# Kernel tuning notes

Measured on AMD Instinct MI355X. Metric: run time of the kernel, lower is better.

## Reference

```python
import jax, jax.numpy as jnp
import numpy as np

N_NODES = 50000


def _gcn_norm(edge_index, num_nodes):
    """PyG GCNConv normalization: add self-loops, symmetric deg^{-1/2} weights."""
    loops = jnp.arange(num_nodes, dtype=edge_index.dtype)
    src = jnp.concatenate([edge_index[0], loops])
    dst = jnp.concatenate([edge_index[1], loops])
    deg = jax.ops.segment_sum(jnp.ones_like(dst, dtype=jnp.float32), dst,
                              num_segments=num_nodes)
    dinv = jax.lax.rsqrt(jnp.maximum(deg, 1.0))  # self-loops guarantee deg>=1
    norm = dinv[src] * dinv[dst]                 # [E + N]
    return src, dst, norm


def _gcn_conv(x, W, b, src, dst, norm, num_nodes):
    h = x @ W                                    # [N, out] dense GEMM
    msg = h[src] * norm[:, None]                 # gather + scale
    agg = jax.ops.segment_sum(msg, dst, num_segments=num_nodes)
    return agg + b


def setup_inputs() -> dict:
    key = jax.random.key(0)
    ks = jax.random.split(key, 8)
    d = 128
    scale = 1.0 / np.sqrt(d)
    emb = jax.random.normal(ks[0], (N_NODES, d), dtype=jnp.float32)
    W1 = jax.random.normal(ks[1], (d, d), dtype=jnp.float32) * scale
    W2 = jax.random.normal(ks[2], (d, d), dtype=jnp.float32) * scale
    W3 = jax.random.normal(ks[3], (d, d), dtype=jnp.float32) * scale
    b1 = jnp.zeros((d,), dtype=jnp.float32)
    b2 = jnp.zeros((d,), dtype=jnp.float32)
    b3 = jnp.zeros((d,), dtype=jnp.float32)
    edge_index = jax.random.randint(ks[4], (2, 600000), 0, N_NODES, dtype=jnp.int64)
    return {"emb": emb, "W1": W1, "b1": b1, "W2": W2, "b2": b2,
            "W3": W3, "b3": b3, "edge_index": edge_index}


def reference(emb, W1, b1, W2, b2, W3, b3, edge_index):
    # Eval-mode forward: F.dropout(training=False) is identity.
    src, dst, norm = _gcn_norm(edge_index, N_NODES)
    x = emb
    x = jax.nn.relu(_gcn_conv(x, W1, b1, src, dst, norm, N_NODES))
    x = jax.nn.relu(_gcn_conv(x, W2, b2, src, dst, norm, N_NODES))
    x = _gcn_conv(x, W3, b3, src, dst, norm, N_NODES)
    x = x.at[0].set(0.0)  # x[0] = zeros(x.shape[1])
    return x
```

## Files before the change

kernel.cpp:

```cpp
#include <hip/hip_runtime.h>
#include <hip/hip_fp16.h>

#define NN 50000
#define D 128
#define STRIDE 64

typedef __attribute__((ext_vector_type(16))) float f32x16;
typedef _Float16 h16;
typedef __attribute__((ext_vector_type(8))) _Float16 h16x8;

struct alignas(16) H8 { h16 h[8]; };

typedef const __attribute__((address_space(1))) void gvoid;
typedef __attribute__((address_space(3))) void lvoid;

__global__ __launch_bounds__(256) void wprep_kernel(const float* __restrict__ W1,
                                                    const float* __restrict__ W2,
                                                    const float* __restrict__ W3,
                                                    h16* __restrict__ Wsp,
                                                    int* __restrict__ cnt) {
    const int b  = blockIdx.x;
    const int w  = b >> 3;
    const int ks = b & 7;
    const float* W = w == 0 ? W1 : (w == 1 ? W2 : W3);
    h16* dst = Wsp + w * 32768;
    const int l  = threadIdx.x & 63;
    const int ct = threadIdx.x >> 6;
    const int n  = ct * 32 + (l & 31);
    const int lh = l >> 5;
    const int kbase = ks * 16 + lh * 8;
    H8 hi8, lo8;
#pragma unroll
    for (int j = 0; j < 8; j++) {
        float wv = W[(kbase + j) * D + n];
        h16 hi = (h16)wv;
        hi8.h[j] = hi;
        lo8.h[j] = (h16)(wv - (float)hi);
    }
    const int base = ((ks * 4 + ct) * 64 + l) * 8;
    *(H8*)(dst + base)         = hi8;
    *(H8*)(dst + base + 16384) = lo8;
    for (int i = b * 256 + threadIdx.x; i < NN; i += 24 * 256) cnt[i] = 0;
}

__global__ __launch_bounds__(256) void fill_kernel(const int* __restrict__ srcA,
                                                   const int* __restrict__ dstA,
                                                   int* __restrict__ cnt,
                                                   int* __restrict__ slots, int noct) {
    int t = blockIdx.x * 256 + threadIdx.x;
    if (t >= noct) return;
    int4 sa = ((const int4*)srcA)[2 * t];
    int4 sb = ((const int4*)srcA)[2 * t + 1];
    int4 da = ((const int4*)dstA)[2 * t];
    int4 db = ((const int4*)dstA)[2 * t + 1];
    int p0 = atomicAdd(&cnt[da.x], 1);
    int p1 = atomicAdd(&cnt[da.y], 1);
    int p2 = atomicAdd(&cnt[da.z], 1);
    int p3 = atomicAdd(&cnt[da.w], 1);
    int p4 = atomicAdd(&cnt[db.x], 1);
    int p5 = atomicAdd(&cnt[db.y], 1);
    int p6 = atomicAdd(&cnt[db.z], 1);
    int p7 = atomicAdd(&cnt[db.w], 1);
    if (p0 < STRIDE - 4) slots[da.x * STRIDE + p0] = sa.x;
    if (p1 < STRIDE - 4) slots[da.y * STRIDE + p1] = sa.y;
    if (p2 < STRIDE - 4) slots[da.z * STRIDE + p2] = sa.z;
    if (p3 < STRIDE - 4) slots[da.w * STRIDE + p3] = sa.w;
    if (p4 < STRIDE - 4) slots[db.x * STRIDE + p4] = sb.x;
    if (p5 < STRIDE - 4) slots[db.y * STRIDE + p5] = sb.y;
    if (p6 < STRIDE - 4) slots[db.z * STRIDE + p6] = sb.z;
    if (p7 < STRIDE - 4) slots[db.w * STRIDE + p7] = sb.w;
}

__global__ __launch_bounds__(256, 2) void gemm_mfma(const void* __restrict__ Xv, int x_is_f32,
                                                    const h16* __restrict__ Wsp,
                                                    h16* __restrict__ H, int M) {
    __shared__ h16 Ws[32768];
    {
        const int t = threadIdx.x;
#pragma unroll
        for (int i = 0; i < 16; i++) {
            const int off = (i * 256 + t) * 8;
            __builtin_amdgcn_global_load_lds((gvoid*)(Wsp + off), (lvoid*)(Ws + off),
                                             16, 0, 0);
        }
    }
    __syncthreads();

    const int wave = threadIdx.x >> 6;
    const int lane = threadIdx.x & 63;
    const int row0 = blockIdx.x * 128 + wave * 32;
    const int arow = min(row0 + (lane & 31), M - 1);
    const int koff = (lane >> 5) * 8;

    f32x16 acc[4] = {};

#pragma unroll
    for (int ks = 0; ks < 8; ks++) {
        h16x8 ahi, alo;
        if (x_is_f32) {
            const float* p = (const float*)Xv + (size_t)arow * D + koff + ks * 16;
            float4 fa = *(const float4*)p;
            float4 fb = *(const float4*)(p + 4);
            float f[8] = {fa.x, fa.y, fa.z, fa.w, fb.x, fb.y, fb.z, fb.w};
#pragma unroll
            for (int j = 0; j < 8; j++) {
                h16 hi = (h16)f[j];
                ahi[j] = hi;
                alo[j] = (h16)(f[j] - (float)hi);
            }
        } else {
            const h16* p = (const h16*)Xv + (size_t)arow * D + koff + ks * 16;
            ahi = *(const h16x8*)p;
        }
#pragma unroll
        for (int ct = 0; ct < 4; ct++) {
            const int base = ((ks * 4 + ct) * 64 + lane) * 8;
            h16x8 bhi = *(const h16x8*)(Ws + base);
            h16x8 blo = *(const h16x8*)(Ws + base + 16384);
            acc[ct] = __builtin_amdgcn_mfma_f32_32x32x16_f16(ahi, bhi, acc[ct], 0, 0, 0);
            acc[ct] = __builtin_amdgcn_mfma_f32_32x32x16_f16(ahi, blo, acc[ct], 0, 0, 0);
            if (x_is_f32)
                acc[ct] = __builtin_amdgcn_mfma_f32_32x32x16_f16(alo, bhi, acc[ct], 0, 0, 0);
        }
    }

    __syncthreads();
    {
        h16* C_lds = Ws;
        const int col0 = lane & 31;
        const int lr0  = 4 * (lane >> 5);
#pragma unroll
        for (int ct = 0; ct < 4; ct++) {
#pragma unroll
            for (int r = 0; r < 16; r++) {
                const int lrow = lr0 + (r & 3) + 8 * (r >> 2);
                C_lds[(wave * 32 + lrow) * D + ct * 32 + col0] = (h16)acc[ct][r];
            }
        }
        const h16* src = C_lds + wave * 32 * D;
        h16* gdst = H + (size_t)row0 * D;
#pragma unroll
        for (int j = 0; j < 8; j++) {
            const int i = j * 64 + lane;
            const int row = row0 + (i >> 4);
            if (row < M)
                *(h16x8*)(gdst + (size_t)i * 8) = *(const h16x8*)(src + i * 8);
        }
    }
}

__global__ __launch_bounds__(256) void agg_kernel(const h16* __restrict__ H,
                                                  const int* __restrict__ cnt,
                                                  const int* __restrict__ slots,
                                                  const float* __restrict__ bias,
                                                  h16* __restrict__ out16,
                                                  float* __restrict__ out32,
                                                  int mode) {
    const int lane = threadIdx.x & 63;
    const int node = blockIdx.x * 4 + (threadIdx.x >> 6);
    const int q    = lane >> 4;
    const int col  = (lane & 15) * 8;

    const int c = __builtin_amdgcn_readfirstlane(cnt[node]);
    const float di = rsqrtf((float)c + 1.0f);
    const int sbase = node * STRIDE;
    const int pc = min((c + 8) & ~7, STRIDE);

    float aA[8] = {0.f, 0.f, 0.f, 0.f, 0.f, 0.f, 0.f, 0.f};
    float aB[8] = {0.f, 0.f, 0.f, 0.f, 0.f, 0.f, 0.f, 0.f};

    int sa = slots[sbase + q];
    int sb = slots[sbase + 4 + q];

    for (int p = 0; p < pc; p += 8) {
        int sa_n = slots[sbase + min(p + 8 + q, STRIDE - 1)];
        int sb_n = slots[sbase + min(p + 12 + q, STRIDE - 1)];
        const int ja = p + q;
        const int jb = p + 4 + q;
        const int ca = (ja < c) ? sa : node;
        const int cb = (jb < c) ? sb : node;
        float wa = (ja < c) ? rsqrtf((float)cnt[ca] + 1.0f) : ((ja == c) ? di : 0.f);
        float wb = (jb < c) ? rsqrtf((float)cnt[cb] + 1.0f) : ((jb == c) ? di : 0.f);
        h16x8 va = *(const h16x8*)(H + (size_t)ca * D + col);
        h16x8 vb = *(const h16x8*)(H + (size_t)cb * D + col);
#pragma unroll
        for (int j = 0; j < 8; j++) {
            aA[j] = fmaf(wa, (float)va[j], aA[j]);
            aB[j] = fmaf(wb, (float)vb[j], aB[j]);
        }
        sa = sa_n; sb = sb_n;
    }

#pragma unroll
    for (int j = 0; j < 8; j++) {
        float v = aA[j] + aB[j];
        v += __shfl_xor(v, 16, 64);
        v += __shfl_xor(v, 32, 64);
        aA[j] = v;
    }

    if (lane < 16) {
        float4 bb0 = *(const float4*)(bias + col);
        float4 bb1 = *(const float4*)(bias + col + 4);
        float r[8];
        r[0] = fmaf(di, aA[0], bb0.x); r[1] = fmaf(di, aA[1], bb0.y);
        r[2] = fmaf(di, aA[2], bb0.z); r[3] = fmaf(di, aA[3], bb0.w);
        r[4] = fmaf(di, aA[4], bb1.x); r[5] = fmaf(di, aA[5], bb1.y);
        r[6] = fmaf(di, aA[6], bb1.z); r[7] = fmaf(di, aA[7], bb1.w);
        if (mode == 0) {
            h16x8 o;
#pragma unroll
            for (int j = 0; j < 8; j++) o[j] = (h16)fmaxf(r[j], 0.f);
            *(h16x8*)(out16 + (size_t)node * D + col) = o;
        } else {
            if (node == 0) {
#pragma unroll
                for (int j = 0; j < 8; j++) r[j] = 0.f;
            }
            *(float4*)(out32 + (size_t)node * D + col)     = make_float4(r[0], r[1], r[2], r[3]);
            *(float4*)(out32 + (size_t)node * D + col + 4) = make_float4(r[4], r[5], r[6], r[7]);
        }
    }
}


extern "C" void kernel_launch(void* const* d_in, const int* in_sizes, int n_in,
                              void* d_out, int out_size, void* d_ws, size_t ws_size,
                              hipStream_t stream) {
    const float* emb = (const float*)d_in[0];
    const float* W1  = (const float*)d_in[1];
    const float* b1  = (const float*)d_in[2];
    const float* W2  = (const float*)d_in[3];
    const float* b2  = (const float*)d_in[4];
    const float* W3  = (const float*)d_in[5];
    const float* b3  = (const float*)d_in[6];
    const int*   ei  = (const int*)d_in[7];

    const int E = in_sizes[7] / 2;
    const int* srcA = ei;
    const int* dstA = ei + E;
    float* out = (float*)d_out;

    char* ws = (char*)d_ws;
    size_t off = 0;
    auto alloc = [&](size_t bytes) -> void* {
        void* p = ws + off;
        off = (off + bytes + 255) & ~(size_t)255;
        return p;
    };
    h16* h      = (h16*)alloc((size_t)NN * D * 2);
    h16* x16    = (h16*)alloc((size_t)NN * D * 2);
    int* cnt    = (int*)alloc((size_t)NN * 4);
    int* slots  = (int*)alloc((size_t)NN * STRIDE * 4);
    h16* Wsp    = (h16*)alloc((size_t)3 * 32768 * 2);

    const int T = 256;
    const int gemm_grid = (NN + 127) / 128;
    const int agg_grid  = NN / 4;
    const int noct = E / 8;

    wprep_kernel<<<24, T, 0, stream>>>(W1, W2, W3, Wsp, cnt);
    gemm_mfma<<<gemm_grid, T, 0, stream>>>(emb, 1, Wsp, h, NN);
    fill_kernel<<<(noct + T - 1) / T, T, 0, stream>>>(srcA, dstA, cnt, slots, noct);
    agg_kernel<<<agg_grid, T, 0, stream>>>(h, cnt, slots, b1, x16, nullptr, 0);
    gemm_mfma<<<gemm_grid, T, 0, stream>>>(x16, 0, Wsp + 32768, h, NN);
    agg_kernel<<<agg_grid, T, 0, stream>>>(h, cnt, slots, b2, x16, nullptr, 0);
    gemm_mfma<<<gemm_grid, T, 0, stream>>>(x16, 0, Wsp + 65536, h, NN);
    agg_kernel<<<agg_grid, T, 0, stream>>>(h, cnt, slots, b3, nullptr, out, 1);
}
```

Measured before the change: 252.1 us.

## Fuse edge-slot fill into first GEMM, enlarge GEMM blocks, batch agg nodes

The separate fill kernel is removed. Its atomic bucketing of edges by destination now runs at the tail of the first GEMM launch, saving one launch. The GEMM moves to 512-thread blocks covering 256 rows, with launch bounds of (512, 4). The aggregation kernel now has each wave process four nodes in turn and hoists the bias load. Risks: the tighter launch bound may force register spills for the 64-float accumulators, and fewer, larger agg blocks may hide memory latency less well.

```diff
diff --git a/kernel.cpp b/kernel.cpp
--- a/kernel.cpp
+++ b/kernel.cpp
@@ -43,43 +43,19 @@
     for (int i = b * 256 + threadIdx.x; i < NN; i += 24 * 256) cnt[i] = 0;
 }
 
-__global__ __launch_bounds__(256) void fill_kernel(const int* __restrict__ srcA,
-                                                   const int* __restrict__ dstA,
-                                                   int* __restrict__ cnt,
-                                                   int* __restrict__ slots, int noct) {
-    int t = blockIdx.x * 256 + threadIdx.x;
-    if (t >= noct) return;
-    int4 sa = ((const int4*)srcA)[2 * t];
-    int4 sb = ((const int4*)srcA)[2 * t + 1];
-    int4 da = ((const int4*)dstA)[2 * t];
-    int4 db = ((const int4*)dstA)[2 * t + 1];
-    int p0 = atomicAdd(&cnt[da.x], 1);
-    int p1 = atomicAdd(&cnt[da.y], 1);
-    int p2 = atomicAdd(&cnt[da.z], 1);
-    int p3 = atomicAdd(&cnt[da.w], 1);
-    int p4 = atomicAdd(&cnt[db.x], 1);
-    int p5 = atomicAdd(&cnt[db.y], 1);
-    int p6 = atomicAdd(&cnt[db.z], 1);
-    int p7 = atomicAdd(&cnt[db.w], 1);
-    if (p0 < STRIDE - 4) slots[da.x * STRIDE + p0] = sa.x;
-    if (p1 < STRIDE - 4) slots[da.y * STRIDE + p1] = sa.y;
-    if (p2 < STRIDE - 4) slots[da.z * STRIDE + p2] = sa.z;
-    if (p3 < STRIDE - 4) slots[da.w * STRIDE + p3] = sa.w;
-    if (p4 < STRIDE - 4) slots[db.x * STRIDE + p4] = sb.x;
-    if (p5 < STRIDE - 4) slots[db.y * STRIDE + p5] = sb.y;
-    if (p6 < STRIDE - 4) slots[db.z * STRIDE + p6] = sb.z;
-    if (p7 < STRIDE - 4) slots[db.w * STRIDE + p7] = sb.w;
-}
-
-__global__ __launch_bounds__(256, 2) void gemm_mfma(const void* __restrict__ Xv, int x_is_f32,
+__global__ __launch_bounds__(512, 4) void gemm_mfma(const void* __restrict__ Xv, int x_is_f32,
                                                     const h16* __restrict__ Wsp,
-                                                    h16* __restrict__ H, int M) {
+                                                    h16* __restrict__ H, int M,
+                                                    const int* __restrict__ srcA,
+                                                    const int* __restrict__ dstA,
+                                                    int* __restrict__ cnt,
+                                                    int* __restrict__ slots, int noct) {
     __shared__ h16 Ws[32768];
     {
         const int t = threadIdx.x;
 #pragma unroll
-        for (int i = 0; i < 16; i++) {
-            const int off = (i * 256 + t) * 8;
+        for (int i = 0; i < 8; i++) {
+            const int off = (i * 512 + t) * 8;
             __builtin_amdgcn_global_load_lds((gvoid*)(Wsp + off), (lvoid*)(Ws + off),
                                              16, 0, 0);
         }
@@ -88,7 +64,7 @@
 
     const int wave = threadIdx.x >> 6;
     const int lane = threadIdx.x & 63;
-    const int row0 = blockIdx.x * 128 + wave * 32;
+    const int row0 = blockIdx.x * 256 + wave * 32;
     const int arow = min(row0 + (lane & 31), M - 1);
     const int koff = (lane >> 5) * 8;
 
@@ -147,6 +123,32 @@
                 *(h16x8*)(gdst + (size_t)i * 8) = *(const h16x8*)(src + i * 8);
         }
     }
+
+    if (srcA) {
+        int t = blockIdx.x * 512 + threadIdx.x;
+        if (t < noct) {
+            int4 sa = ((const int4*)srcA)[2 * t];
+            int4 sb = ((const int4*)srcA)[2 * t + 1];
+            int4 da = ((const int4*)dstA)[2 * t];
+            int4 db = ((const int4*)dstA)[2 * t + 1];
+            int p0 = atomicAdd(&cnt[da.x], 1);
+            int p1 = atomicAdd(&cnt[da.y], 1);
+            int p2 = atomicAdd(&cnt[da.z], 1);
+            int p3 = atomicAdd(&cnt[da.w], 1);
+            int p4 = atomicAdd(&cnt[db.x], 1);
+            int p5 = atomicAdd(&cnt[db.y], 1);
+            int p6 = atomicAdd(&cnt[db.z], 1);
+            int p7 = atomicAdd(&cnt[db.w], 1);
+            if (p0 < STRIDE - 4) slots[da.x * STRIDE + p0] = sa.x;
+            if (p1 < STRIDE - 4) slots[da.y * STRIDE + p1] = sa.y;
+            if (p2 < STRIDE - 4) slots[da.z * STRIDE + p2] = sa.z;
+            if (p3 < STRIDE - 4) slots[da.w * STRIDE + p3] = sa.w;
+            if (p4 < STRIDE - 4) slots[db.x * STRIDE + p4] = sb.x;
+            if (p5 < STRIDE - 4) slots[db.y * STRIDE + p5] = sb.y;
+            if (p6 < STRIDE - 4) slots[db.z * STRIDE + p6] = sb.z;
+            if (p7 < STRIDE - 4) slots[db.w * STRIDE + p7] = sb.w;
+        }
+    }
 }
 
 __global__ __launch_bounds__(256) void agg_kernel(const h16* __restrict__ H,
@@ -156,69 +158,73 @@
                                                   h16* __restrict__ out16,
                                                   float* __restrict__ out32,
                                                   int mode) {
-    const int lane = threadIdx.x & 63;
-    const int node = blockIdx.x * 4 + (threadIdx.x >> 6);
-    const int q    = lane >> 4;
-    const int col  = (lane & 15) * 8;
-
-    const int c = __builtin_amdgcn_readfirstlane(cnt[node]);
-    const float di = rsqrtf((float)c + 1.0f);
-    const int sbase = node * STRIDE;
-    const int pc = min((c + 8) & ~7, STRIDE);
-
-    float aA[8] = {0.f, 0.f, 0.f, 0.f, 0.f, 0.f, 0.f, 0.f};
-    float aB[8] = {0.f, 0.f, 0.f, 0.f, 0.f, 0.f, 0.f, 0.f};
-
-    int sa = slots[sbase + q];
-    int sb = slots[sbase + 4 + q];
-
-    for (int p = 0; p < pc; p += 8) {
-        int sa_n = slots[sbase + min(p + 8 + q, STRIDE - 1)];
-        int sb_n = slots[sbase + min(p + 12 + q, STRIDE - 1)];
-        const int ja = p + q;
-        const int jb = p + 4 + q;
-        const int ca = (ja < c) ? sa : node;
-        const int cb = (jb < c) ? sb : node;
-        float wa = (ja < c) ? rsqrtf((float)cnt[ca] + 1.0f) : ((ja == c) ? di : 0.f);
-        float wb = (jb < c) ? rsqrtf((float)cnt[cb] + 1.0f) : ((jb == c) ? di : 0.f);
-        h16x8 va = *(const h16x8*)(H + (size_t)ca * D + col);
-        h16x8 vb = *(const h16x8*)(H + (size_t)cb * D + col);
+    const int lane  = threadIdx.x & 63;
+    const int q     = lane >> 4;
+    const int col   = (lane & 15) * 8;
+    const int node0 = blockIdx.x * 16 + (threadIdx.x >> 6) * 4;
+
+    const float4 bb0 = *(const float4*)(bias + col);
+    const float4 bb1 = *(const float4*)(bias + col + 4);
+
+    for (int nn = 0; nn < 4; nn++) {
+        const int node = node0 + nn;
+        const int c = __builtin_amdgcn_readfirstlane(cnt[node]);
+        const float di = rsqrtf((float)c + 1.0f);
+        const int sbase = node * STRIDE;
+        const int pc = min((c + 8) & ~7, STRIDE);
+
+        float aA[8] = {0.f, 0.f, 0.f, 0.f, 0.f, 0.f, 0.f, 0.f};
+        float aB[8] = {0.f, 0.f, 0.f, 0.f, 0.f, 0.f, 0.f, 0.f};
+
+        int sa = slots[sbase + q];
+        int sb = slots[sbase + 4 + q];
+
+        for (int p = 0; p < pc; p += 8) {
+            int sa_n = slots[sbase + min(p + 8 + q, STRIDE - 1)];
+            int sb_n = slots[sbase + min(p + 12 + q, STRIDE - 1)];
+            const int ja = p + q;
+            const int jb = p + 4 + q;
+            const int ca = (ja < c) ? sa : node;
+            const int cb = (jb < c) ? sb : node;
+            float wa = (ja < c) ? rsqrtf((float)cnt[ca] + 1.0f) : ((ja == c) ? di : 0.f);
+            float wb = (jb < c) ? rsqrtf((float)cnt[cb] + 1.0f) : ((jb == c) ? di : 0.f);
+            h16x8 va = *(const h16x8*)(H + (size_t)ca * D + col);
+            h16x8 vb = *(const h16x8*)(H + (size_t)cb * D + col);
+#pragma unroll
+            for (int j = 0; j < 8; j++) {
+                aA[j] = fmaf(wa, (float)va[j], aA[j]);
+                aB[j] = fmaf(wb, (float)vb[j], aB[j]);
+            }
+            sa = sa_n; sb = sb_n;
+        }
+
 #pragma unroll
         for (int j = 0; j < 8; j++) {
-            aA[j] = fmaf(wa, (float)va[j], aA[j]);
-            aB[j] = fmaf(wb, (float)vb[j], aB[j]);
-        }
-        sa = sa_n; sb = sb_n;
-    }
-
-#pragma unroll
-    for (int j = 0; j < 8; j++) {
-        float v = aA[j] + aB[j];
-        v += __shfl_xor(v, 16, 64);
-        v += __shfl_xor(v, 32, 64);
-        aA[j] = v;
-    }
-
-    if (lane < 16) {
-        float4 bb0 = *(const float4*)(bias + col);
-        float4 bb1 = *(const float4*)(bias + col + 4);
-        float r[8];
-        r[0] = fmaf(di, aA[0], bb0.x); r[1] = fmaf(di, aA[1], bb0.y);
-        r[2] = fmaf(di, aA[2], bb0.z); r[3] = fmaf(di, aA[3], bb0.w);
-        r[4] = fmaf(di, aA[4], bb1.x); r[5] = fmaf(di, aA[5], bb1.y);
-        r[6] = fmaf(di, aA[6], bb1.z); r[7] = fmaf(di, aA[7], bb1.w);
-        if (mode == 0) {
-            h16x8 o;
-#pragma unroll
-            for (int j = 0; j < 8; j++) o[j] = (h16)fmaxf(r[j], 0.f);
-            *(h16x8*)(out16 + (size_t)node * D + col) = o;
-        } else {
-            if (node == 0) {
-#pragma unroll
-                for (int j = 0; j < 8; j++) r[j] = 0.f;
-            }
-            *(float4*)(out32 + (size_t)node * D + col)     = make_float4(r[0], r[1], r[2], r[3]);
-            *(float4*)(out32 + (size_t)node * D + col + 4) = make_float4(r[4], r[5], r[6], r[7]);
+            float v = aA[j] + aB[j];
+            v += __shfl_xor(v, 16, 64);
+            v += __shfl_xor(v, 32, 64);
+            aA[j] = v;
+        }
+
+        if (lane < 16) {
+            float r[8];
+            r[0] = fmaf(di, aA[0], bb0.x); r[1] = fmaf(di, aA[1], bb0.y);
+            r[2] = fmaf(di, aA[2], bb0.z); r[3] = fmaf(di, aA[3], bb0.w);
+            r[4] = fmaf(di, aA[4], bb1.x); r[5] = fmaf(di, aA[5], bb1.y);
+            r[6] = fmaf(di, aA[6], bb1.z); r[7] = fmaf(di, aA[7], bb1.w);
+            if (mode == 0) {
+                h16x8 o;
+#pragma unroll
+                for (int j = 0; j < 8; j++) o[j] = (h16)fmaxf(r[j], 0.f);
+                *(h16x8*)(out16 + (size_t)node * D + col) = o;
+            } else {
+                if (node == 0) {
+#pragma unroll
+                    for (int j = 0; j < 8; j++) r[j] = 0.f;
+                }
+                *(float4*)(out32 + (size_t)node * D + col)     = make_float4(r[0], r[1], r[2], r[3]);
+                *(float4*)(out32 + (size_t)node * D + col + 4) = make_float4(r[4], r[5], r[6], r[7]);
+            }
         }
     }
 }
@@ -254,17 +260,18 @@
     int* slots  = (int*)alloc((size_t)NN * STRIDE * 4);
     h16* Wsp    = (h16*)alloc((size_t)3 * 32768 * 2);
 
-    const int T = 256;
-    const int gemm_grid = (NN + 127) / 128;
-    const int agg_grid  = NN / 4;
+    const int gemm_grid = (NN + 255) / 256;
+    const int agg_grid  = NN / 16;
     const int noct = E / 8;
 
-    wprep_kernel<<<24, T, 0, stream>>>(W1, W2, W3, Wsp, cnt);
-    gemm_mfma<<<gemm_grid, T, 0, stream>>>(emb, 1, Wsp, h, NN);
-    fill_kernel<<<(noct + T - 1) / T, T, 0, stream>>>(srcA, dstA, cnt, slots, noct);
-    agg_kernel<<<agg_grid, T, 0, stream>>>(h, cnt, slots, b1, x16, nullptr, 0);
-    gemm_mfma<<<gemm_grid, T, 0, stream>>>(x16, 0, Wsp + 32768, h, NN);
-    agg_kernel<<<agg_grid, T, 0, stream>>>(h, cnt, slots, b2, x16, nullptr, 0);
-    gemm_mfma<<<gemm_grid, T, 0, stream>>>(x16, 0, Wsp + 65536, h, NN);
-    agg_kernel<<<agg_grid, T, 0, stream>>>(h, cnt, slots, b3, nullptr, out, 1);
-}
+    wprep_kernel<<<24, 256, 0, stream>>>(W1, W2, W3, Wsp, cnt);
+    gemm_mfma<<<gemm_grid, 512, 0, stream>>>(emb, 1, Wsp, h, NN,
+                                             srcA, dstA, cnt, slots, noct);
+    agg_kernel<<<agg_grid, 256, 0, stream>>>(h, cnt, slots, b1, x16, nullptr, 0);
+    gemm_mfma<<<gemm_grid, 512, 0, stream>>>(x16, 0, Wsp + 32768, h, NN,
+                                             nullptr, nullptr, nullptr, nullptr, 0);
+    agg_kernel<<<agg_grid, 256, 0, stream>>>(h, cnt, slots, b2, x16, nullptr, 0);
+    gemm_mfma<<<gemm_grid, 512, 0, stream>>>(x16, 0, Wsp + 65536, h, NN,
+                                             nullptr, nullptr, nullptr, nullptr, 0);
+    agg_kernel<<<agg_grid, 256, 0, stream>>>(h, cnt, slots, b3, nullptr, out, 1);
+}
```

Result: faster. 246.0 us (-2.4%).
